# Kernel tuning notes

Hardware: AMD Instinct MI355X
Metric: run time of the kernel (lower is better)

Reference implementation:

```python
import jax, jax.numpy as jnp
import numpy as np

HIDDEN = 768
NHEADS = 12
HEAD = HIDDEN // NHEADS


def setup_inputs() -> dict:
    key = jax.random.key(0)
    ks = jax.random.split(key, 10)
    B, S = 32, 512
    s = 1.0 / np.sqrt(HIDDEN)
    return {
        "x": jax.random.normal(ks[0], (B, S, HIDDEN), jnp.float32),
        "additive_attention_mask": jnp.zeros((B, 1, 1, S), jnp.float32),
        "Wq": jax.random.normal(ks[1], (HIDDEN, HIDDEN), jnp.float32) * s,
        "bq": jnp.zeros((HIDDEN,), jnp.float32),
        "Wk": jax.random.normal(ks[2], (HIDDEN, HIDDEN), jnp.float32) * s,
        "bk": jnp.zeros((HIDDEN,), jnp.float32),
        "Wv": jax.random.normal(ks[3], (HIDDEN, HIDDEN), jnp.float32) * s,
        "bv": jnp.zeros((HIDDEN,), jnp.float32),
        "Wo": jax.random.normal(ks[4], (HIDDEN, HIDDEN), jnp.float32) * s,
        "bo": jnp.zeros((HIDDEN,), jnp.float32),
    }


def reference(x, additive_attention_mask, Wq, bq, Wk, bk, Wv, bv, Wo, bo):
    B, S, _ = x.shape
    # projections (dropout is identity in eval mode)
    q = (x @ Wq + bq).reshape(B, S, NHEADS, HEAD)
    k = (x @ Wk + bk).reshape(B, S, NHEADS, HEAD)
    v = (x @ Wv + bv).reshape(B, S, NHEADS, HEAD)
    scores = jnp.einsum('bqhd,bkhd->bhqk', q, k) / jnp.sqrt(jnp.float32(HEAD))
    scores = scores + additive_attention_mask  # broadcast [B,1,1,S]
    probs = jax.nn.softmax(scores, axis=-1)
    attn = jnp.einsum('bhqk,bkhd->bqhd', probs, v).reshape(B, S, HIDDEN)
    return attn @ Wo + bo
```

## Files before the change

### kernel.cpp

```cpp
#include <hip/hip_runtime.h>
#include <stdint.h>

typedef unsigned short u16;
typedef __attribute__((ext_vector_type(4))) float floatx4;
typedef __attribute__((ext_vector_type(8))) __bf16 bf16x8;

__device__ __forceinline__ u16 f2bf(float f) {
  uint32_t u = __float_as_uint(f);
  u += 0x7FFFu + ((u >> 16) & 1u);
  return (u16)(u >> 16);
}

__global__ __launch_bounds__(256) void cast_x_kernel(const float* __restrict__ x,
                                                     u16* __restrict__ out) {
  int i = blockIdx.x * 256 + threadIdx.x;
  const float4* p = (const float4*)x;
  float4 a = p[(size_t)i * 2];
  float4 b = p[(size_t)i * 2 + 1];
  uint32_t w0 = (uint32_t)f2bf(a.x) | ((uint32_t)f2bf(a.y) << 16);
  uint32_t w1 = (uint32_t)f2bf(a.z) | ((uint32_t)f2bf(a.w) << 16);
  uint32_t w2 = (uint32_t)f2bf(b.x) | ((uint32_t)f2bf(b.y) << 16);
  uint32_t w3 = (uint32_t)f2bf(b.z) | ((uint32_t)f2bf(b.w) << 16);
  *(uint4*)(out + (size_t)i * 8) = make_uint4(w0, w1, w2, w3);
}

__global__ __launch_bounds__(256) void prep_w_kernel(
    const float* __restrict__ Wq, const float* __restrict__ Wk,
    const float* __restrict__ Wv, const float* __restrict__ Wo,
    const float* __restrict__ bq, const float* __restrict__ bk, const float* __restrict__ bv,
    u16* __restrict__ Wt, u16* __restrict__ Wto, float* __restrict__ bias) {
  __shared__ u16 sT[64][72];
  const int kt = blockIdx.x * 64, nt = blockIdx.y * 64, mat = blockIdx.z;
  const float* W = mat == 0 ? Wq : mat == 1 ? Wk : mat == 2 ? Wv : Wo;
  const int tid = threadIdx.x;
  const int r = tid >> 2, c4 = tid & 3;
#pragma unroll
  for (int p = 0; p < 4; ++p) {
    int c = c4 * 16 + p * 4;
    float4 v = *(const float4*)&W[(size_t)(kt + r) * 768 + nt + c];
    sT[c + 0][r] = f2bf(v.x);
    sT[c + 1][r] = f2bf(v.y);
    sT[c + 2][r] = f2bf(v.z);
    sT[c + 3][r] = f2bf(v.w);
  }
  __syncthreads();
  const int n = tid >> 2, kq = tid & 3;
  uint4 o0 = *(const uint4*)&sT[n][kq * 16];
  uint4 o1 = *(const uint4*)&sT[n][kq * 16 + 8];
  u16* dst = (mat < 3 ? Wt + ((size_t)(mat * 768 + nt + n)) * 768
                      : Wto + (size_t)(nt + n) * 768) + kt + kq * 16;
  *(uint4*)dst = o0;
  *(uint4*)(dst + 8) = o1;
  if (mat < 3 && blockIdx.x == 0 && tid < 64) {
    const float* bs = mat == 0 ? bq : mat == 1 ? bk : bv;
    bias[mat * 768 + nt + tid] = bs[nt + tid];
  }
}

__device__ __forceinline__ void gload16(const void* g, void* l) {
  __builtin_amdgcn_global_load_lds((const __attribute__((address_space(1))) void*)g,
                                   (__attribute__((address_space(3))) void*)l,
                                   16, 0, 0);
}

template <int OUTF32>
__global__ __launch_bounds__(256, 4) void gemm_bt_kernel(
    const u16* __restrict__ A, const u16* __restrict__ Bt,
    const float* __restrict__ bias, void* __restrict__ Cv, int ldc) {
  __shared__ __align__(16) u16 Alds[128 * 64];
  __shared__ __align__(16) u16 Blds[128 * 64];
  const int m0 = blockIdx.x * 128, n0 = blockIdx.y * 128;
  const int tid = threadIdx.x;
  const int lane = tid & 63, wid = tid >> 6;
  const int wr = wid >> 1, wc = wid & 1;
  const int l15 = lane & 15, l4 = lane >> 4;
  const int srow = lane >> 3;
  const int csw = (lane & 7) ^ srow;

  floatx4 zz = {0.f, 0.f, 0.f, 0.f};
  floatx4 acc[4][4];
#pragma unroll
  for (int i = 0; i < 4; ++i)
#pragma unroll
    for (int j = 0; j < 4; ++j) acc[i][j] = zz;

  for (int kt = 0; kt < 768; kt += 64) {
#pragma unroll
    for (int i = 0; i < 4; ++i) {
      int u = wid * 4 + i;
      int row = u * 8 + srow;
      gload16(A + (size_t)(m0 + row) * 768 + kt + csw * 8, (char*)Alds + u * 1024);
      gload16(Bt + (size_t)(n0 + row) * 768 + kt + csw * 8, (char*)Blds + u * 1024);
    }
    __syncthreads();
#pragma unroll
    for (int kk = 0; kk < 2; ++kk) {
      bf16x8 af[4], bfr[4];
#pragma unroll
      for (int i = 0; i < 4; ++i) {
        int ra = wr * 64 + i * 16 + l15;
        int rb = wc * 64 + i * 16 + l15;
        af[i]  = *(const bf16x8*)((char*)Alds + ra * 128 + (((kk * 4 + l4) ^ (l15 & 7)) << 4));
        bfr[i] = *(const bf16x8*)((char*)Blds + rb * 128 + (((kk * 4 + l4) ^ (l15 & 7)) << 4));
      }
#pragma unroll
      for (int i = 0; i < 4; ++i)
#pragma unroll
        for (int j = 0; j < 4; ++j)
          acc[i][j] = __builtin_amdgcn_mfma_f32_16x16x32_bf16(af[i], bfr[j], acc[i][j], 0, 0, 0);
    }
    __syncthreads();
  }

#pragma unroll
  for (int i = 0; i < 4; ++i) {
    int row = m0 + wr * 64 + i * 16 + l4 * 4;
#pragma unroll
    for (int j = 0; j < 4; ++j) {
      int col = n0 + wc * 64 + j * 16 + l15;
      float bv = bias[col];
#pragma unroll
      for (int r = 0; r < 4; ++r) {
        float v = acc[i][j][r] + bv;
        if (OUTF32) ((float*)Cv)[(size_t)(row + r) * ldc + col] = v;
        else        ((u16*)Cv)[(size_t)(row + r) * ldc + col] = f2bf(v);
      }
    }
  }
}

__global__ __launch_bounds__(512, 4) void attn_kernel(const u16* __restrict__ qkv,
                                                      const float* __restrict__ mask,
                                                      u16* __restrict__ ctx) {
  __shared__ __align__(16) char lds[34816];
  char* sK = lds;
  char* sV = lds + 16384;
  float* sM = (float*)(lds + 32768);

  const int bid = blockIdx.x;
  const int wg = (bid & 7) * 192 + (bid >> 3);
  const int qt = wg & 3;
  const int h = (wg >> 2) % 12;
  const int b = wg / 48;

  const int tid = threadIdx.x;
  const int lane = tid & 63, w = tid >> 6;
  const int l15 = lane & 15, l4 = lane >> 4;
  const int hi = lane >> 3, doct = lane & 7;

  const u16* base = qkv + (size_t)b * 512 * 2304 + h * 64;
  const u16* Qg = base;
  const u16* Kg = base + 768;
  const u16* Vg = base + 1536;

  const int csw = doct ^ hi;
  const int vp_ = w * 8 + hi;

  auto stageK = [&](int t) {
    const u16* src = Kg + (size_t)(t * 128 + w * 16) * 2304;
#pragma unroll
    for (int i = 0; i < 2; ++i)
      gload16(src + (size_t)(i * 8 + hi) * 2304 + csw * 8,
              sK + (w * 2 + i) * 1024);
  };
  uint4 vra, vrb;
  auto loadV = [&](int t) {
    const u16* vp = Vg + (size_t)(t * 128 + vp_ * 2) * 2304 + doct * 8;
    vra = *(const uint4*)vp;
    vrb = *(const uint4*)(vp + 2304);
  };
  auto writeV = [&]() {
    const u16* pa = (const u16*)&vra;
    const u16* pb = (const u16*)&vrb;
#pragma unroll
    for (int j = 0; j < 8; ++j) {
      int d = doct * 8 + j;
      uint32_t val = (uint32_t)pa[j] | ((uint32_t)pb[j] << 16);
      *(uint32_t*)(sV + d * 256 +
                   ((4 * vp_) ^ ((d & 7) << 4) ^ (((d >> 3) & 3) << 5))) = val;
    }
  };

  float mval = mask[(size_t)b * 512 + tid];
  stageK(0);
  loadV(0);
  const u16* qp = Qg + (size_t)(qt * 128 + w * 16 + l15) * 2304 + l4 * 8;
  bf16x8 qf0 = *(const bf16x8*)qp;
  bf16x8 qf1 = *(const bf16x8*)(qp + 32);
  sM[tid] = mval;
  writeV();
  asm volatile("s_waitcnt vmcnt(0) lgkmcnt(0)" ::: "memory");
  __builtin_amdgcn_sched_barrier(0);
  __builtin_amdgcn_s_barrier();

  floatx4 zz = {0.f, 0.f, 0.f, 0.f};
  floatx4 oacc[4];
#pragma unroll
  for (int da = 0; da < 4; ++da) oacc[da] = zz;
  float m_ = -1e30f, l_ = 0.f;

  const int kswz = (l15 & 7) << 4;
  const int src0 = l15 + 32 * (l4 & 1);
  const int src1 = src0 + 16;
  const bool csel = (l4 & 2) != 0;

  for (int t = 0; t < 4; ++t) {
    if (t < 3) loadV(t + 1);

    floatx4 sacc[8];
#pragma unroll
    for (int ct = 0; ct < 8; ++ct) sacc[ct] = zz;
#pragma unroll
    for (int ct = 0; ct < 8; ++ct) {
      const char* kr = sK + (ct * 16 + l15) * 128;
      bf16x8 k0 = *(const bf16x8*)(kr + ((16 * l4) ^ kswz));
      bf16x8 k1 = *(const bf16x8*)(kr + ((64 + 16 * l4) ^ kswz));
      sacc[ct] = __builtin_amdgcn_mfma_f32_16x16x32_bf16(k0, qf0, sacc[ct], 0, 0, 0);
      sacc[ct] = __builtin_amdgcn_mfma_f32_16x16x32_bf16(k1, qf1, sacc[ct], 0, 0, 0);
    }

    float pm = -1e30f;
#pragma unroll
    for (int ct = 0; ct < 8; ++ct) {
      floatx4 mv = *(const floatx4*)(sM + t * 128 + ct * 16 + l4 * 4);
#pragma unroll
      for (int j = 0; j < 4; ++j) {
        float v = sacc[ct][j] * 0.125f + mv[j];
        sacc[ct][j] = v;
        pm = fmaxf(pm, v);
      }
    }
    pm = fmaxf(pm, __shfl_xor(pm, 16, 64));
    pm = fmaxf(pm, __shfl_xor(pm, 32, 64));
    float nm = fmaxf(m_, pm);
    float sc = __expf(m_ - nm);
    m_ = nm;
    float ts = 0.f;
#pragma unroll
    for (int ct = 0; ct < 8; ++ct)
#pragma unroll
      for (int j = 0; j < 4; ++j) {
        float e = __expf(sacc[ct][j] - nm);
        sacc[ct][j] = e;
        ts += e;
      }
    ts += __shfl_xor(ts, 16, 64);
    ts += __shfl_xor(ts, 32, 64);
    l_ = l_ * sc + ts;
#pragma unroll
    for (int da = 0; da < 4; ++da)
#pragma unroll
      for (int j = 0; j < 4; ++j) oacc[da][j] *= sc;

    uint32_t pk[8][2];
#pragma unroll
    for (int ct = 0; ct < 8; ++ct) {
#pragma unroll
      for (int p = 0; p < 2; ++p) {
        uint32_t ua = __float_as_uint(sacc[ct][2 * p]) + 0x8000u;
        uint32_t ub = __float_as_uint(sacc[ct][2 * p + 1]) + 0x8000u;
        pk[ct][p] = (ua >> 16) | (ub & 0xFFFF0000u);
      }
    }

#pragma unroll
    for (int ks = 0; ks < 4; ++ks) {
      uint32_t A0 = __shfl((int)pk[2 * ks][0], src0, 64);
      uint32_t B0 = __shfl((int)pk[2 * ks + 1][0], src0, 64);
      uint32_t A1 = __shfl((int)pk[2 * ks][1], src0, 64);
      uint32_t B1 = __shfl((int)pk[2 * ks + 1][1], src0, 64);
      uint32_t A2 = __shfl((int)pk[2 * ks][0], src1, 64);
      uint32_t B2 = __shfl((int)pk[2 * ks + 1][0], src1, 64);
      uint32_t A3 = __shfl((int)pk[2 * ks][1], src1, 64);
      uint32_t B3 = __shfl((int)pk[2 * ks + 1][1], src1, 64);
      union { uint32_t u[4]; bf16x8 v; } pf;
      pf.u[0] = csel ? B0 : A0;
      pf.u[1] = csel ? B1 : A1;
      pf.u[2] = csel ? B2 : A2;
      pf.u[3] = csel ? B3 : A3;
#pragma unroll
      for (int da = 0; da < 4; ++da) {
        int dd = da * 16 + l15;
        bf16x8 vf = *(const bf16x8*)(sV + dd * 256 +
            ((64 * ks + 16 * l4) ^ ((dd & 7) << 4) ^ (((dd >> 3) & 3) << 5)));
        oacc[da] = __builtin_amdgcn_mfma_f32_16x16x32_bf16(vf, pf.v, oacc[da], 0, 0, 0);
      }
    }

    asm volatile("s_waitcnt lgkmcnt(0)" ::: "memory");
    __builtin_amdgcn_sched_barrier(0);
    __builtin_amdgcn_s_barrier();
    if (t < 3) {
      stageK(t + 1);
      writeV();
      asm volatile("s_waitcnt vmcnt(0) lgkmcnt(0)" ::: "memory");
      __builtin_amdgcn_sched_barrier(0);
      __builtin_amdgcn_s_barrier();
    }
  }

  float rl = 1.0f / l_;
  u16* op = ctx + ((size_t)b * 512 + qt * 128 + w * 16 + l15) * 768 + h * 64;
#pragma unroll
  for (int da = 0; da < 4; ++da) {
    ushort4 o;
    o.x = f2bf(oacc[da][0] * rl);
    o.y = f2bf(oacc[da][1] * rl);
    o.z = f2bf(oacc[da][2] * rl);
    o.w = f2bf(oacc[da][3] * rl);
    *(ushort4*)(op + da * 16 + l4 * 4) = o;
  }
}

extern "C" void kernel_launch(void* const* d_in, const int* in_sizes, int n_in,
                              void* d_out, int out_size, void* d_ws, size_t ws_size,
                              hipStream_t stream) {
  const float* x    = (const float*)d_in[0];
  const float* mask = (const float*)d_in[1];
  const float* Wq   = (const float*)d_in[2];
  const float* bq   = (const float*)d_in[3];
  const float* Wk   = (const float*)d_in[4];
  const float* bk   = (const float*)d_in[5];
  const float* Wv   = (const float*)d_in[6];
  const float* bv   = (const float*)d_in[7];
  const float* Wo   = (const float*)d_in[8];
  const float* bo   = (const float*)d_in[9];
  float* out = (float*)d_out;

  char* ws = (char*)d_ws;
  u16*   xb   = (u16*)ws;
  u16*   ctx  = (u16*)(ws + 25165824);
  u16*   qkv  = (u16*)(ws + 50331648);
  u16*   wtq  = (u16*)(ws + 125829120);
  u16*   wto  = (u16*)(ws + 129368064);
  float* bqkv = (float*)(ws + 130547712);

  cast_x_kernel<<<6144, 256, 0, stream>>>(x, xb);
  prep_w_kernel<<<dim3(12, 12, 4), 256, 0, stream>>>(Wq, Wk, Wv, Wo, bq, bk, bv,
                                                     wtq, wto, bqkv);
  gemm_bt_kernel<0><<<dim3(128, 18), 256, 0, stream>>>(xb, wtq, bqkv, (void*)qkv, 2304);
  attn_kernel<<<dim3(1536), dim3(512), 0, stream>>>(qkv, mask, ctx);
  gemm_bt_kernel<1><<<dim3(128, 6), 256, 0, stream>>>(ctx, wto, bo, (void*)out, 768);
}
```

Baseline: 162.0 us.

## Double-buffer K tiles in attention and add lazy softmax rescaling

After: 166.4 us. 1.03x slower.

```diff
diff --git a/kernel.cpp b/kernel.cpp
--- a/kernel.cpp
+++ b/kernel.cpp
@@ -132,10 +132,10 @@
 __global__ __launch_bounds__(512, 4) void attn_kernel(const u16* __restrict__ qkv,
                                                       const float* __restrict__ mask,
                                                       u16* __restrict__ ctx) {
-  __shared__ __align__(16) char lds[34816];
+  __shared__ __align__(16) char lds[51200];
   char* sK = lds;
-  char* sV = lds + 16384;
-  float* sM = (float*)(lds + 32768);
+  char* sV = lds + 32768;
+  float* sM = (float*)(lds + 49152);
 
   const int bid = blockIdx.x;
   const int wg = (bid & 7) * 192 + (bid >> 3);
@@ -156,12 +156,12 @@
   const int csw = doct ^ hi;
   const int vp_ = w * 8 + hi;
 
-  auto stageK = [&](int t) {
+  auto stageK = [&](int t, int kb) {
     const u16* src = Kg + (size_t)(t * 128 + w * 16) * 2304;
 #pragma unroll
     for (int i = 0; i < 2; ++i)
       gload16(src + (size_t)(i * 8 + hi) * 2304 + csw * 8,
-              sK + (w * 2 + i) * 1024);
+              sK + kb * 16384 + (w * 2 + i) * 1024);
   };
   uint4 vra, vrb;
   auto loadV = [&](int t) {
@@ -182,14 +182,15 @@
   };
 
   float mval = mask[(size_t)b * 512 + tid];
-  stageK(0);
+  stageK(0, 0);
   loadV(0);
   const u16* qp = Qg + (size_t)(qt * 128 + w * 16 + l15) * 2304 + l4 * 8;
   bf16x8 qf0 = *(const bf16x8*)qp;
   bf16x8 qf1 = *(const bf16x8*)(qp + 32);
   sM[tid] = mval;
+  asm volatile("s_waitcnt vmcnt(0)" ::: "memory");
   writeV();
-  asm volatile("s_waitcnt vmcnt(0) lgkmcnt(0)" ::: "memory");
+  asm volatile("s_waitcnt lgkmcnt(0)" ::: "memory");
   __builtin_amdgcn_sched_barrier(0);
   __builtin_amdgcn_s_barrier();
 
@@ -204,100 +205,97 @@
   const int src1 = src0 + 16;
   const bool csel = (l4 & 2) != 0;
 
-  for (int t = 0; t < 4; ++t) {
-    if (t < 3) loadV(t + 1);
-
-    floatx4 sacc[8];
-#pragma unroll
-    for (int ct = 0; ct < 8; ++ct) sacc[ct] = zz;
-#pragma unroll
-    for (int ct = 0; ct < 8; ++ct) {
-      const char* kr = sK + (ct * 16 + l15) * 128;
-      bf16x8 k0 = *(const bf16x8*)(kr + ((16 * l4) ^ kswz));
-      bf16x8 k1 = *(const bf16x8*)(kr + ((64 + 16 * l4) ^ kswz));
-      sacc[ct] = __builtin_amdgcn_mfma_f32_16x16x32_bf16(k0, qf0, sacc[ct], 0, 0, 0);
-      sacc[ct] = __builtin_amdgcn_mfma_f32_16x16x32_bf16(k1, qf1, sacc[ct], 0, 0, 0);
-    }
-
-    float pm = -1e30f;
-#pragma unroll
-    for (int ct = 0; ct < 8; ++ct) {
-      floatx4 mv = *(const floatx4*)(sM + t * 128 + ct * 16 + l4 * 4);
-#pragma unroll
-      for (int j = 0; j < 4; ++j) {
-        float v = sacc[ct][j] * 0.125f + mv[j];
-        sacc[ct][j] = v;
-        pm = fmaxf(pm, v);
-      }
-    }
-    pm = fmaxf(pm, __shfl_xor(pm, 16, 64));
-    pm = fmaxf(pm, __shfl_xor(pm, 32, 64));
-    float nm = fmaxf(m_, pm);
-    float sc = __expf(m_ - nm);
-    m_ = nm;
-    float ts = 0.f;
-#pragma unroll
-    for (int ct = 0; ct < 8; ++ct)
-#pragma unroll
-      for (int j = 0; j < 4; ++j) {
-        float e = __expf(sacc[ct][j] - nm);
-        sacc[ct][j] = e;
-        ts += e;
-      }
-    ts += __shfl_xor(ts, 16, 64);
-    ts += __shfl_xor(ts, 32, 64);
-    l_ = l_ * sc + ts;
-#pragma unroll
-    for (int da = 0; da < 4; ++da)
-#pragma unroll
-      for (int j = 0; j < 4; ++j) oacc[da][j] *= sc;
-
-    uint32_t pk[8][2];
-#pragma unroll
-    for (int ct = 0; ct < 8; ++ct) {
-#pragma unroll
-      for (int p = 0; p < 2; ++p) {
-        uint32_t ua = __float_as_uint(sacc[ct][2 * p]) + 0x8000u;
-        uint32_t ub = __float_as_uint(sacc[ct][2 * p + 1]) + 0x8000u;
-        pk[ct][p] = (ua >> 16) | (ub & 0xFFFF0000u);
-      }
-    }
-
-#pragma unroll
-    for (int ks = 0; ks < 4; ++ks) {
-      uint32_t A0 = __shfl((int)pk[2 * ks][0], src0, 64);
-      uint32_t B0 = __shfl((int)pk[2 * ks + 1][0], src0, 64);
-      uint32_t A1 = __shfl((int)pk[2 * ks][1], src0, 64);
-      uint32_t B1 = __shfl((int)pk[2 * ks + 1][1], src0, 64);
-      uint32_t A2 = __shfl((int)pk[2 * ks][0], src1, 64);
-      uint32_t B2 = __shfl((int)pk[2 * ks + 1][0], src1, 64);
-      uint32_t A3 = __shfl((int)pk[2 * ks][1], src1, 64);
-      uint32_t B3 = __shfl((int)pk[2 * ks + 1][1], src1, 64);
-      union { uint32_t u[4]; bf16x8 v; } pf;
-      pf.u[0] = csel ? B0 : A0;
-      pf.u[1] = csel ? B1 : A1;
-      pf.u[2] = csel ? B2 : A2;
-      pf.u[3] = csel ? B3 : A3;
-#pragma unroll
-      for (int da = 0; da < 4; ++da) {
-        int dd = da * 16 + l15;
-        bf16x8 vf = *(const bf16x8*)(sV + dd * 256 +
-            ((64 * ks + 16 * l4) ^ ((dd & 7) << 4) ^ (((dd >> 3) & 3) << 5)));
-        oacc[da] = __builtin_amdgcn_mfma_f32_16x16x32_bf16(vf, pf.v, oacc[da], 0, 0, 0);
-      }
-    }
-
-    asm volatile("s_waitcnt lgkmcnt(0)" ::: "memory");
-    __builtin_amdgcn_sched_barrier(0);
-    __builtin_amdgcn_s_barrier();
-    if (t < 3) {
-      stageK(t + 1);
-      writeV();
-      asm volatile("s_waitcnt vmcnt(0) lgkmcnt(0)" ::: "memory");
-      __builtin_amdgcn_sched_barrier(0);
-      __builtin_amdgcn_s_barrier();
-    }
-  }
+#define COMPUTE(T, DOTRANS)                                                           \
+  {                                                                                   \
+    if (DOTRANS) { stageK((T) + 1, ((T) + 1) & 1); loadV((T) + 1); }                  \
+    const char* sKb = sK + ((T) & 1) * 16384;                                         \
+    floatx4 sacc[8];                                                                  \
+    _Pragma("unroll") for (int ct = 0; ct < 8; ++ct) sacc[ct] = zz;                   \
+    _Pragma("unroll") for (int ct = 0; ct < 8; ++ct) {                                \
+      const char* kr = sKb + (ct * 16 + l15) * 128;                                   \
+      bf16x8 k0 = *(const bf16x8*)(kr + ((16 * l4) ^ kswz));                          \
+      bf16x8 k1 = *(const bf16x8*)(kr + ((64 + 16 * l4) ^ kswz));                     \
+      sacc[ct] = __builtin_amdgcn_mfma_f32_16x16x32_bf16(k0, qf0, sacc[ct], 0, 0, 0); \
+      sacc[ct] = __builtin_amdgcn_mfma_f32_16x16x32_bf16(k1, qf1, sacc[ct], 0, 0, 0); \
+    }                                                                                 \
+    float pm = -1e30f;                                                                \
+    _Pragma("unroll") for (int ct = 0; ct < 8; ++ct) {                                \
+      floatx4 mv = *(const floatx4*)(sM + (T) * 128 + ct * 16 + l4 * 4);              \
+      _Pragma("unroll") for (int j = 0; j < 4; ++j) {                                 \
+        float v = sacc[ct][j] * 0.125f + mv[j];                                       \
+        sacc[ct][j] = v;                                                              \
+        pm = fmaxf(pm, v);                                                            \
+      }                                                                               \
+    }                                                                                 \
+    pm = fmaxf(pm, __shfl_xor(pm, 16, 64));                                           \
+    pm = fmaxf(pm, __shfl_xor(pm, 32, 64));                                           \
+    if (__any(pm > m_ + 8.f)) {       \
+      float nm = fmaxf(m_, pm);                                                       \
+      float sc = __expf(m_ - nm);                                                     \
+      m_ = nm;                                                                        \
+      l_ *= sc;                                                                       \
+      _Pragma("unroll") for (int da = 0; da < 4; ++da)                                \
+        _Pragma("unroll") for (int j = 0; j < 4; ++j) oacc[da][j] *= sc;              \
+    }                                                                                 \
+    float ts = 0.f;                                                                   \
+    _Pragma("unroll") for (int ct = 0; ct < 8; ++ct)                                  \
+      _Pragma("unroll") for (int j = 0; j < 4; ++j) {                                 \
+        float e = __expf(sacc[ct][j] - m_);                                           \
+        sacc[ct][j] = e;                                                              \
+        ts += e;                                                                      \
+      }                                                                               \
+    ts += __shfl_xor(ts, 16, 64);                                                     \
+    ts += __shfl_xor(ts, 32, 64);                                                     \
+    l_ += ts;                                                                         \
+    uint32_t pk[8][2];                                                                \
+    _Pragma("unroll") for (int ct = 0; ct < 8; ++ct) {                                \
+      union { uint32_t u[2]; __bf16 hh[4]; } cv;                                      \
+      cv.hh[0] = (__bf16)sacc[ct][0];                                                 \
+      cv.hh[1] = (__bf16)sacc[ct][1];                                                 \
+      cv.hh[2] = (__bf16)sacc[ct][2];                                                 \
+      cv.hh[3] = (__bf16)sacc[ct][3];                                                 \
+      pk[ct][0] = cv.u[0];                                                            \
+      pk[ct][1] = cv.u[1];                                                            \
+    }                                                                                 \
+    _Pragma("unroll") for (int ks = 0; ks < 4; ++ks) {                                \
+      uint32_t A0 = __shfl((int)pk[2 * ks][0], src0, 64);                             \
+      uint32_t B0 = __shfl((int)pk[2 * ks + 1][0], src0, 64);                         \
+      uint32_t A1 = __shfl((int)pk[2 * ks][1], src0, 64);                             \
+      uint32_t B1 = __shfl((int)pk[2 * ks + 1][1], src0, 64);                         \
+      uint32_t A2 = __shfl((int)pk[2 * ks][0], src1, 64);                             \
+      uint32_t B2 = __shfl((int)pk[2 * ks + 1][0], src1, 64);                         \
+      uint32_t A3 = __shfl((int)pk[2 * ks][1], src1, 64);                             \
+      uint32_t B3 = __shfl((int)pk[2 * ks + 1][1], src1, 64);                         \
+      union { uint32_t u[4]; bf16x8 v; } pf;                                          \
+      pf.u[0] = csel ? B0 : A0;                                                       \
+      pf.u[1] = csel ? B1 : A1;                                                       \
+      pf.u[2] = csel ? B2 : A2;                                                       \
+      pf.u[3] = csel ? B3 : A3;                                                       \
+      _Pragma("unroll") for (int da = 0; da < 4; ++da) {                              \
+        int dd = da * 16 + l15;                                                       \
+        bf16x8 vf = *(const bf16x8*)(sV + dd * 256 +                                  \
+            ((64 * ks + 16 * l4) ^ ((dd & 7) << 4) ^ (((dd >> 3) & 3) << 5)));        \
+        oacc[da] = __builtin_amdgcn_mfma_f32_16x16x32_bf16(vf, pf.v, oacc[da], 0, 0, 0); \
+      }                                                                               \
+    }                                                                                 \
+    if (DOTRANS) {                                                                    \
+      asm volatile("s_waitcnt lgkmcnt(0)" ::: "memory");                              \
+      __builtin_amdgcn_sched_barrier(0);                                              \
+      __builtin_amdgcn_s_barrier();                 \
+      asm volatile("s_waitcnt vmcnt(0)" ::: "memory");        \
+      __builtin_amdgcn_sched_barrier(0);                                              \
+      writeV();                                                                       \
+      asm volatile("s_waitcnt lgkmcnt(0)" ::: "memory");                              \
+      __builtin_amdgcn_sched_barrier(0);                                              \
+      __builtin_amdgcn_s_barrier();                    \
+    }                                                                                 \
+  }
+
+  COMPUTE(0, 1)
+  COMPUTE(1, 1)
+  COMPUTE(2, 1)
+  COMPUTE(3, 0)
+#undef COMPUTE
 
   float rl = 1.0f / l_;
   u16* op = ctx + ((size_t)b * 512 + qt * 128 + w * 16 + l15) * 768 + h * 64;
```
